# Kernel tuning notes

Hardware: AMD Instinct MI355X
Metric: run time of the kernel (lower is better)

## Reference

```python
import jax, jax.numpy as jnp
import numpy as np


def _block(x, a, b):
    # [..., W, H, D] -> [..., W//a, H//b, a, b, D]
    w, h, d = x.shape[-3:]
    x = jnp.reshape(x, x.shape[:-3] + (w // a, a, h // b, b, d))
    return jnp.moveaxis(x, -4, -3)


def _combine(x, bs):
    # [..., W, H, D] -> [..., W//bs, H//bs, bs*bs*D]
    x = _block(x, bs, bs)
    return jnp.reshape(x, x.shape[:-3] + (-1,))


def _normalize(x):
    x = x - jnp.mean(x, axis=-1, keepdims=True)
    return x / (jnp.linalg.norm(x, axis=-1, keepdims=True) + 1e-05)


def setup_inputs() -> dict:
    key = jax.random.key(0)
    k1, k2 = jax.random.split(key)
    x = jax.random.normal(k1, (8, 128, 128, 64), dtype=jnp.float32)
    y = jax.random.normal(k2, (8, 128, 128, 64), dtype=jnp.float32)
    return {"x": x, "y": y, "blocksize": 4}


def reference(x, y, blocksize):
    shape = x.shape
    xc = _normalize(_combine(x, blocksize))  # [B, W/bs, H/bs, F]
    yc = _normalize(_combine(y, blocksize))
    yf = jnp.reshape(yc, (-1, yc.shape[-1]))  # [M, F] codebook
    # single similarity matrix, reused for min-loss and argmax (original
    # computed jnp.inner twice -- same math)
    sim = jnp.einsum('...f,mf->...m', xc, yf)  # [B, W/bs, H/bs, M]
    cosloss = jnp.mean(jnp.min(1.0 - sim, axis=-1))
    idx = jnp.argmax(sim, axis=-1)
    # one-hot matmul against yf == top-1 gather (argmax picks first max, as
    # does the original I = (argmax - arange == 0) construction)
    new_x = jnp.take(yf, idx, axis=0)  # [B, W/bs, H/bs, F]
    new_x = jnp.reshape(new_x, new_x.shape[:-1] + (blocksize, blocksize, -1))
    new_x = jnp.swapaxes(new_x, -4, -3)
    new_x = jnp.reshape(new_x, shape)
    return cosloss, new_x
```

## Files before the change

kernel.cpp:

```cpp
#include <hip/hip_runtime.h>
#include <math.h>


#define NROWS 8192
#define KY 1024
#define NCH 64
#define EPS 3e-4f
#define FEPS 8e-4f

typedef _Float16 v8h __attribute__((ext_vector_type(8)));
typedef float f32x4 __attribute__((ext_vector_type(4)));

__device__ __forceinline__ unsigned umax(unsigned a, unsigned b) { return a > b ? a : b; }
__device__ __forceinline__ unsigned umin(unsigned a, unsigned b) { return a < b ? a : b; }

__device__ __forceinline__ unsigned packKey(float v, int col) {
    unsigned b = __float_as_uint(v);
    b ^= (unsigned)((int)b >> 31) | 0x80000000u;
    return (b & 0xFFFFE000u) | (unsigned)(8191 - col);
}

__device__ __forceinline__ float unpackApprox(unsigned k) {
    unsigned kb = k & 0xFFFFE000u;
    unsigned b = (kb & 0x80000000u) ? (kb ^ 0x80000000u) : ~kb;
    return __uint_as_float(b);
}

#define KMERGE(a1, a2, a3, b1, b2, b3) do {                                 \
    unsigned _n1 = umax(a1, b1);                                            \
    unsigned _n2 = umax(umin(a1, b1), umax(a2, b2));                        \
    unsigned _n3 = umax(umax(a3, b3), umax(umin(a1, b2), umin(a2, b1)));    \
    a1 = _n1; a2 = _n2; a3 = _n3;                                           \
} while (0)

__global__ __launch_bounds__(256) void normSplitKernel(
    const float* __restrict__ x, const float* __restrict__ y,
    _Float16* __restrict__ Xh, _Float16* __restrict__ Xl,
    _Float16* __restrict__ Yh, _Float16* __restrict__ Yl,
    int* __restrict__ flagCnt) {
    if (blockIdx.x == 0 && threadIdx.x == 0) *flagCnt = 0;
    int gr = blockIdx.x * 4 + (threadIdx.x >> 6);
    int ln = threadIdx.x & 63;
    bool isX = gr < NROWS;
    int row = isX ? gr : gr - NROWS;
    const float* src = isX ? x : y;
    _Float16* dh = isX ? Xh : Yh;
    _Float16* dl = isX ? Xl : Yl;
    int b = row >> 10, wq = (row >> 5) & 31, hq = row & 31;
    int a = ln >> 4, c = (ln >> 2) & 3, d0 = (ln & 3) << 4;
    const float* p = &src[(((size_t)(b * 128) + wq * 4 + a) * 128 + hq * 4 + c) * 64 + d0];
    float vv[16];
    *(float4*)(vv + 0)  = *(const float4*)(p + 0);
    *(float4*)(vv + 4)  = *(const float4*)(p + 4);
    *(float4*)(vv + 8)  = *(const float4*)(p + 8);
    *(float4*)(vv + 12) = *(const float4*)(p + 12);
    double s = 0.0;
    #pragma unroll
    for (int q = 0; q < 16; q++) s += (double)vv[q];
    #pragma unroll
    for (int m = 1; m < 64; m <<= 1) s += __shfl_xor(s, m, 64);
    double mean = s * (1.0 / 1024.0);
    double ss = 0.0;
    #pragma unroll
    for (int q = 0; q < 16; q++) {
        double d = (double)vv[q] - mean;
        ss += d * d;
    }
    #pragma unroll
    for (int m = 1; m < 64; m <<= 1) ss += __shfl_xor(ss, m, 64);
    double scale = 1.0 / (sqrt(ss) + 1e-5);
    _Float16 hi[16], lo[16];
    #pragma unroll
    for (int q = 0; q < 16; q++) {
        float f = (float)(((double)vv[q] - mean) * scale);
        _Float16 h = (_Float16)f;
        hi[q] = h;
        lo[q] = (_Float16)(f - (float)h);
    }
    size_t f0 = (size_t)row * KY + (ln << 4);
    *(v8h*)&dh[f0]     = *(v8h*)(hi);
    *(v8h*)&dh[f0 + 8] = *(v8h*)(hi + 8);
    *(v8h*)&dl[f0]     = *(v8h*)(lo);
    *(v8h*)&dl[f0 + 8] = *(v8h*)(lo + 8);
}

__global__ __launch_bounds__(256) void simKernel(
    const _Float16* __restrict__ Xh, const _Float16* __restrict__ Yh,
    float* __restrict__ pV1, unsigned* __restrict__ pK1,
    unsigned* __restrict__ pK2, unsigned* __restrict__ pK3) {
    __shared__ _Float16 As[2][128 * 32];
    __shared__ _Float16 Bs[2][128 * 32];
    __shared__ unsigned sK[2][2][64][3];
    __shared__ float sE[2][2][64];
    const int t = threadIdx.x;
    const int l = t & 63, w = t >> 6;
    const int wr = w >> 1, wc = w & 1;
    const int quad = l >> 4, lm = l & 15;
    const int flat = blockIdx.y * 64 + blockIdx.x;
    const int bx = flat >> 6, by = flat & 63;
    const int r0 = bx * 128, c0 = by * 128;

    f32x4 acc[4][4];
    #pragma unroll
    for (int i = 0; i < 4; i++)
        #pragma unroll
        for (int j = 0; j < 4; j++) acc[i][j] = (f32x4){0.f, 0.f, 0.f, 0.f};

    const _Float16* srcA0 = Xh + (size_t)(r0 + (t >> 2)) * KY + ((t & 3) << 3);
    const _Float16* srcA1 = srcA0 + (size_t)64 * KY;
    const _Float16* srcB0 = Yh + (size_t)(c0 + (t >> 2)) * KY + ((t & 3) << 3);
    const _Float16* srcB1 = srcB0 + (size_t)64 * KY;
    const int st8 = t * 8;

    {
        uint4 a0 = *(const uint4*)srcA0;
        uint4 a1 = *(const uint4*)srcA1;
        uint4 b0 = *(const uint4*)srcB0;
        uint4 b1 = *(const uint4*)srcB1;
        *(uint4*)&As[0][st8] = a0;
        *(uint4*)&As[0][2048 + st8] = a1;
        *(uint4*)&Bs[0][st8] = b0;
        *(uint4*)&Bs[0][2048 + st8] = b1;
    }
    __syncthreads();

    const int offA0 = (wr * 64 + lm) * 32 + quad * 8;
    const int offB0 = (wc * 64 + lm) * 32 + quad * 8;

    #pragma unroll 1
    for (int kk = 0; kk < KY - 32; kk += 32) {
        const int cur = (kk >> 5) & 1, nxt = cur ^ 1;
        const int kn = kk + 32;
        uint4 na0 = *(const uint4*)(srcA0 + kn);
        uint4 na1 = *(const uint4*)(srcA1 + kn);
        uint4 nb0 = *(const uint4*)(srcB0 + kn);
        uint4 nb1 = *(const uint4*)(srcB1 + kn);
        v8h af[4], bf[4];
        #pragma unroll
        for (int i = 0; i < 4; i++)
            af[i] = *(const v8h*)&As[cur][offA0 + i * 512];
        #pragma unroll
        for (int j = 0; j < 4; j++)
            bf[j] = *(const v8h*)&Bs[cur][offB0 + j * 512];
        #pragma unroll
        for (int i = 0; i < 4; i++)
            #pragma unroll
            for (int j = 0; j < 4; j++)
                acc[i][j] = __builtin_amdgcn_mfma_f32_16x16x32_f16(af[i], bf[j], acc[i][j], 0, 0, 0);
        *(uint4*)&As[nxt][st8] = na0;
        *(uint4*)&As[nxt][2048 + st8] = na1;
        *(uint4*)&Bs[nxt][st8] = nb0;
        *(uint4*)&Bs[nxt][2048 + st8] = nb1;
        __syncthreads();
    }
    {
        v8h af[4], bf[4];
        #pragma unroll
        for (int i = 0; i < 4; i++)
            af[i] = *(const v8h*)&As[1][offA0 + i * 512];
        #pragma unroll
        for (int j = 0; j < 4; j++)
            bf[j] = *(const v8h*)&Bs[1][offB0 + j * 512];
        #pragma unroll
        for (int i = 0; i < 4; i++)
            #pragma unroll
            for (int j = 0; j < 4; j++)
                acc[i][j] = __builtin_amdgcn_mfma_f32_16x16x32_f16(af[i], bf[j], acc[i][j], 0, 0, 0);
    }

    const int cbase = c0 + wc * 64 + lm;
    #pragma unroll
    for (int i = 0; i < 4; i++) {
        #pragma unroll
        for (int r = 0; r < 4; r++) {
            float v0 = acc[i][0][r], v1 = acc[i][1][r];
            float v2 = acc[i][2][r], v3 = acc[i][3][r];
            unsigned k0 = packKey(v0, cbase);
            unsigned k1 = packKey(v1, cbase + 16);
            unsigned k2 = packKey(v2, cbase + 32);
            unsigned k3 = packKey(v3, cbase + 48);
            unsigned h1 = umax(k0, k1), l1 = umin(k0, k1);
            unsigned h2 = umax(k2, k3), l2 = umin(k2, k3);
            unsigned a1 = umax(h1, h2);
            unsigned a2 = umax(umin(h1, h2), umax(l1, l2));
            unsigned a3 = umax(umin(h1, l2), umin(l1, h2));
            float ev = fmaxf(fmaxf(v0, v1), fmaxf(v2, v3));
            #pragma unroll
            for (int m = 1; m < 16; m <<= 1) {
                unsigned b1 = (unsigned)__shfl_xor((int)a1, m, 64);
                unsigned b2 = (unsigned)__shfl_xor((int)a2, m, 64);
                unsigned b3 = (unsigned)__shfl_xor((int)a3, m, 64);
                float be = __shfl_xor(ev, m, 64);
                KMERGE(a1, a2, a3, b1, b2, b3);
                ev = fmaxf(ev, be);
            }
            if (lm == 0) {
                int rr = i * 16 + quad * 4 + r;
                sK[wr][wc][rr][0] = a1; sK[wr][wc][rr][1] = a2; sK[wr][wc][rr][2] = a3;
                sE[wr][wc][rr] = ev;
            }
        }
    }
    __syncthreads();
    if (wc == 0) {
        unsigned a1 = sK[wr][0][l][0], a2 = sK[wr][0][l][1], a3 = sK[wr][0][l][2];
        unsigned b1 = sK[wr][1][l][0], b2 = sK[wr][1][l][1], b3 = sK[wr][1][l][2];
        KMERGE(a1, a2, a3, b1, b2, b3);
        float ev = fmaxf(sE[wr][0][l], sE[wr][1][l]);
        size_t o = (size_t)by * NROWS + (r0 + wr * 64 + l);
        pV1[o] = ev;
        pK1[o] = a1; pK2[o] = a2; pK3[o] = a3;
    }
}

__global__ __launch_bounds__(256) void reduceKernel(
    const float* __restrict__ pV1, const unsigned* __restrict__ pK1,
    const unsigned* __restrict__ pK2, const unsigned* __restrict__ pK3,
    int* __restrict__ bestIdx, int* __restrict__ flagRows,
    int* __restrict__ flagC2, int* __restrict__ flagC3,
    int* __restrict__ flagCnt, float* __restrict__ blkSum) {
    int t = threadIdx.x;
    int row = blockIdx.x * 256 + t;
    unsigned a1 = 0, a2 = 0, a3 = 0;
    float ev = -1e30f;
    for (int c = 0; c < NCH; c++) {
        size_t o = (size_t)c * NROWS + row;
        unsigned b1 = pK1[o], b2 = pK2[o], b3 = pK3[o];
        float e = pV1[o];
        KMERGE(a1, a2, a3, b1, b2, b3);
        ev = fmaxf(ev, e);
    }
    bestIdx[row] = 8191 - (int)(a1 & 8191u);
    if (ev - unpackApprox(a2) < FEPS) {
        int s = atomicAdd(flagCnt, 1);
        flagRows[s] = row;
        flagC2[s] = 8191 - (int)(a2 & 8191u);
        flagC3[s] = 8191 - (int)(a3 & 8191u);
    }
    double sum = 1.0 - (double)ev;
    __shared__ double sh[4];
    #pragma unroll
    for (int off = 32; off; off >>= 1) sum += __shfl_down(sum, off, 64);
    if ((t & 63) == 0) sh[t >> 6] = sum;
    __syncthreads();
    if (t == 0) blkSum[blockIdx.x] = (float)(sh[0] + sh[1] + sh[2] + sh[3]);
}

__global__ __launch_bounds__(256) void refineKernel(
    const _Float16* __restrict__ Xh, const _Float16* __restrict__ Xl,
    const _Float16* __restrict__ Yh, const _Float16* __restrict__ Yl,
    int* __restrict__ bestIdx, const int* __restrict__ flagRows,
    const int* __restrict__ flagC2, const int* __restrict__ flagC3,
    const int* __restrict__ flagCnt) {
    int n = *flagCnt;
    int wave = (blockIdx.x << 2) + (threadIdx.x >> 6);
    int ln = threadIdx.x & 63;
    for (int fi = wave; fi < n; fi += gridDim.x * 4) {
        int row = flagRows[fi];
        int cand[3];
        cand[0] = bestIdx[row]; cand[1] = flagC2[fi]; cand[2] = flagC3[fi];
        double d[3];
        #pragma unroll
        for (int c = 0; c < 3; c++) {
            double p = 0.0;
            int yr = cand[c];
            #pragma unroll
            for (int q = 0; q < 16; q++) {
                int k = (ln << 4) + q;
                float xv = (float)Xh[(size_t)row * KY + k] + (float)Xl[(size_t)row * KY + k];
                float yv = (float)Yh[(size_t)yr * KY + k] + (float)Yl[(size_t)yr * KY + k];
                p += (double)xv * yv;
            }
            #pragma unroll
            for (int m = 1; m < 64; m <<= 1) p += __shfl_xor(p, m, 64);
            d[c] = p;
        }
        if (ln == 0) {
            int bi = cand[0]; double bv = d[0];
            #pragma unroll
            for (int c = 1; c < 3; c++) {
                if (d[c] > bv || (d[c] == bv && cand[c] < bi)) { bv = d[c]; bi = cand[c]; }
            }
            bestIdx[row] = bi;
        }
    }
}

__global__ __launch_bounds__(256) void gatherKernel(
    const _Float16* __restrict__ Yh, const _Float16* __restrict__ Yl,
    const int* __restrict__ bestIdx, const float* __restrict__ blkSum,
    float* __restrict__ out) {
    int t = threadIdx.x;
    if (blockIdx.x == 0 && t == 0) {
        double s = 0.0;
        for (int i = 0; i < 32; i++) s += (double)blkSum[i];
        out[0] = (float)(s / 8192.0);
    }
    int g = (blockIdx.x * 256 + t) << 2;
    int b = g >> 20, wq = (g >> 13) & 127, hq = (g >> 6) & 127, d = g & 63;
    int row = (b << 10) + ((wq >> 2) << 5) + (hq >> 2);
    int f = ((wq & 3) << 8) + ((hq & 3) << 6) + d;
    size_t base = (size_t)bestIdx[row] * KY + f;
    const _Float16* ph = &Yh[base];
    const _Float16* pl = &Yl[base];
    out[1 + g + 0] = (float)ph[0] + (float)pl[0];
    out[1 + g + 1] = (float)ph[1] + (float)pl[1];
    out[1 + g + 2] = (float)ph[2] + (float)pl[2];
    out[1 + g + 3] = (float)ph[3] + (float)pl[3];
}

extern "C" void kernel_launch(void* const* d_in, const int* in_sizes, int n_in,
                              void* d_out, int out_size, void* d_ws, size_t ws_size,
                              hipStream_t stream) {
    const float* x = (const float*)d_in[0];
    const float* y = (const float*)d_in[1];
    float* out = (float*)d_out;
    char* ws = (char*)d_ws;
    _Float16* Xh  = (_Float16*)(ws);
    _Float16* Xl  = (_Float16*)(ws + 16777216u);
    _Float16* Yh  = (_Float16*)(ws + 33554432u);
    _Float16* Yl  = (_Float16*)(ws + 50331648u);
    float* pV1    = (float*)(ws + 67108864u);
    unsigned* pK1 = (unsigned*)(ws + 69206016u);
    unsigned* pK2 = (unsigned*)(ws + 71303168u);
    unsigned* pK3 = (unsigned*)(ws + 73400320u);
    int* bestIdx  = (int*)  (ws + 79691776u);
    int* flagRows = (int*)  (ws + 79724544u);
    int* flagC2   = (int*)  (ws + 79757312u);
    int* flagC3   = (int*)  (ws + 79790080u);
    int* flagCnt  = (int*)  (ws + 79822848u);
    float* blkSum = (float*)(ws + 79822976u);

    normSplitKernel<<<4096, 256, 0, stream>>>(x, y, Xh, Xl, Yh, Yl, flagCnt);
    simKernel<<<dim3(64, 64), 256, 0, stream>>>(Xh, Yh, pV1, pK1, pK2, pK3);
    reduceKernel<<<32, 256, 0, stream>>>(pV1, pK1, pK2, pK3,
                                         bestIdx, flagRows, flagC2, flagC3, flagCnt, blkSum);
    refineKernel<<<64, 256, 0, stream>>>(Xh, Xl, Yh, Yl, bestIdx,
                                         flagRows, flagC2, flagC3, flagCnt);
    gatherKernel<<<8192, 256, 0, stream>>>(Yh, Yl, bestIdx, blkSum, out);
}
```

Measured before the change: 356.4 us.

## Enlarge GEMM tiles to 256x256 with direct-to-LDS loads and swizzle

The similarity GEMM moves from 128x128 tiles with 256 threads to 256x256 tiles with 512 threads. Each wave computes a 128x64 sub-tile, which raises the reuse of each loaded fragment. Global-to-shared copies now use the global_load_lds intrinsic with an XOR swizzle, double buffering and explicit waitcnt/barrier scheduling plus setprio around the MFMA block. The number of column partials drops to 32, so the reduce kernel is reworked to use 4 lanes per row with shuffle merges across 128 blocks, and the final loss sum covers 128 block sums. The costs are higher register and LDS pressure and hand-written synchronisation that is fragile.

```diff
diff --git a/kernel.cpp b/kernel.cpp
--- a/kernel.cpp
+++ b/kernel.cpp
@@ -4,12 +4,18 @@
 
 #define NROWS 8192
 #define KY 1024
-#define NCH 64
+#define NCH 32
 #define EPS 3e-4f
 #define FEPS 8e-4f
 
 typedef _Float16 v8h __attribute__((ext_vector_type(8)));
 typedef float f32x4 __attribute__((ext_vector_type(4)));
+
+__device__ __forceinline__ void gload16(const _Float16* g, _Float16* l) {
+    __builtin_amdgcn_global_load_lds(
+        (const __attribute__((address_space(1))) void*)g,
+        (__attribute__((address_space(3))) void*)l, 16, 0, 0);
+}
 
 __device__ __forceinline__ unsigned umax(unsigned a, unsigned b) { return a > b ? a : b; }
 __device__ __forceinline__ unsigned umin(unsigned a, unsigned b) { return a < b ? a : b; }
@@ -84,93 +90,79 @@
     *(v8h*)&dl[f0 + 8] = *(v8h*)(lo + 8);
 }
 
-__global__ __launch_bounds__(256) void simKernel(
+__global__ __launch_bounds__(512, 2) void simKernel(
     const _Float16* __restrict__ Xh, const _Float16* __restrict__ Yh,
     float* __restrict__ pV1, unsigned* __restrict__ pK1,
     unsigned* __restrict__ pK2, unsigned* __restrict__ pK3) {
-    __shared__ _Float16 As[2][128 * 32];
-    __shared__ _Float16 Bs[2][128 * 32];
-    __shared__ unsigned sK[2][2][64][3];
-    __shared__ float sE[2][2][64];
+    __shared__ __align__(16) _Float16 As[2][256 * 32];
+    __shared__ __align__(16) _Float16 Bs[2][256 * 32];
+    __shared__ unsigned sK[2][4][128][3];
+    __shared__ float sE[2][4][128];
     const int t = threadIdx.x;
     const int l = t & 63, w = t >> 6;
-    const int wr = w >> 1, wc = w & 1;
+    const int wr = w >> 2, wc = w & 3;
     const int quad = l >> 4, lm = l & 15;
-    const int flat = blockIdx.y * 64 + blockIdx.x;
-    const int bx = flat >> 6, by = flat & 63;
-    const int r0 = bx * 128, c0 = by * 128;
-
-    f32x4 acc[4][4];
-    #pragma unroll
-    for (int i = 0; i < 4; i++)
+    const int flat = blockIdx.x;
+    const int bx = flat >> 5, by = flat & 31;
+    const int r0 = bx * 256, c0 = by * 256;
+
+    f32x4 acc[8][4];
+    #pragma unroll
+    for (int i = 0; i < 8; i++)
         #pragma unroll
         for (int j = 0; j < 4; j++) acc[i][j] = (f32x4){0.f, 0.f, 0.f, 0.f};
 
-    const _Float16* srcA0 = Xh + (size_t)(r0 + (t >> 2)) * KY + ((t & 3) << 3);
-    const _Float16* srcA1 = srcA0 + (size_t)64 * KY;
-    const _Float16* srcB0 = Yh + (size_t)(c0 + (t >> 2)) * KY + ((t & 3) << 3);
-    const _Float16* srcB1 = srcB0 + (size_t)64 * KY;
-    const int st8 = t * 8;
-
-    {
-        uint4 a0 = *(const uint4*)srcA0;
-        uint4 a1 = *(const uint4*)srcA1;
-        uint4 b0 = *(const uint4*)srcB0;
-        uint4 b1 = *(const uint4*)srcB1;
-        *(uint4*)&As[0][st8] = a0;
-        *(uint4*)&As[0][2048 + st8] = a1;
-        *(uint4*)&Bs[0][st8] = b0;
-        *(uint4*)&Bs[0][2048 + st8] = b1;
-    }
-    __syncthreads();
-
-    const int offA0 = (wr * 64 + lm) * 32 + quad * 8;
-    const int offB0 = (wc * 64 + lm) * 32 + quad * 8;
-
-    #pragma unroll 1
-    for (int kk = 0; kk < KY - 32; kk += 32) {
-        const int cur = (kk >> 5) & 1, nxt = cur ^ 1;
-        const int kn = kk + 32;
-        uint4 na0 = *(const uint4*)(srcA0 + kn);
-        uint4 na1 = *(const uint4*)(srcA1 + kn);
-        uint4 nb0 = *(const uint4*)(srcB0 + kn);
-        uint4 nb1 = *(const uint4*)(srcB1 + kn);
-        v8h af[4], bf[4];
-        #pragma unroll
-        for (int i = 0; i < 4; i++)
-            af[i] = *(const v8h*)&As[cur][offA0 + i * 512];
+    const int cq = l >> 2;
+    const int sA = (((l & 3) ^ (cq & 3)) << 3);
+    const _Float16* gA = Xh + (size_t)(r0 + w * 16 + cq) * KY + sA;
+    const _Float16* gB = Yh + (size_t)(c0 + w * 16 + cq) * KY + sA;
+    const int ldsBase = w * 512;
+
+#define STAGE(bb, kt) do {                                             \
+    const int _ko = (kt) * 32;                                         \
+    gload16(gA + _ko,                     &As[bb][ldsBase]);           \
+    gload16(gA + _ko + (size_t)128 * KY,  &As[bb][ldsBase + 4096]);    \
+    gload16(gB + _ko,                     &Bs[bb][ldsBase]);           \
+    gload16(gB + _ko + (size_t)128 * KY,  &Bs[bb][ldsBase + 4096]);    \
+} while (0)
+
+    const int swz = (quad ^ (lm & 3)) << 3;
+    const int offA0 = (wr * 128 + lm) * 32 + swz;
+    const int offB0 = (wc * 64 + lm) * 32 + swz;
+
+    STAGE(0, 0);
+    STAGE(1, 1);
+    asm volatile("s_waitcnt vmcnt(4)" ::: "memory");
+    __builtin_amdgcn_s_barrier();
+
+    #pragma unroll 2
+    for (int kt = 0; kt < 32; kt++) {
+        const int cur = kt & 1;
+        v8h af[8], bf[4];
+        #pragma unroll
+        for (int i = 0; i < 8; i++) af[i] = *(const v8h*)&As[cur][offA0 + i * 512];
+        #pragma unroll
+        for (int j = 0; j < 4; j++) bf[j] = *(const v8h*)&Bs[cur][offB0 + j * 512];
+        asm volatile("s_waitcnt lgkmcnt(0)" ::: "memory");
+        __builtin_amdgcn_sched_barrier(0);
+        __builtin_amdgcn_s_barrier();
+        STAGE(cur, (kt + 2) & 31);
+        __builtin_amdgcn_s_setprio(1);
         #pragma unroll
         for (int j = 0; j < 4; j++)
-            bf[j] = *(const v8h*)&Bs[cur][offB0 + j * 512];
-        #pragma unroll
-        for (int i = 0; i < 4; i++)
-            #pragma unroll
-            for (int j = 0; j < 4; j++)
+            #pragma unroll
+            for (int i = 0; i < 8; i++)
                 acc[i][j] = __builtin_amdgcn_mfma_f32_16x16x32_f16(af[i], bf[j], acc[i][j], 0, 0, 0);
-        *(uint4*)&As[nxt][st8] = na0;
-        *(uint4*)&As[nxt][2048 + st8] = na1;
-        *(uint4*)&Bs[nxt][st8] = nb0;
-        *(uint4*)&Bs[nxt][2048 + st8] = nb1;
-        __syncthreads();
-    }
-    {
-        v8h af[4], bf[4];
-        #pragma unroll
-        for (int i = 0; i < 4; i++)
-            af[i] = *(const v8h*)&As[1][offA0 + i * 512];
-        #pragma unroll
-        for (int j = 0; j < 4; j++)
-            bf[j] = *(const v8h*)&Bs[1][offB0 + j * 512];
-        #pragma unroll
-        for (int i = 0; i < 4; i++)
-            #pragma unroll
-            for (int j = 0; j < 4; j++)
-                acc[i][j] = __builtin_amdgcn_mfma_f32_16x16x32_f16(af[i], bf[j], acc[i][j], 0, 0, 0);
-    }
+        __builtin_amdgcn_s_setprio(0);
+        asm volatile("s_waitcnt vmcnt(4)" ::: "memory");
+        __builtin_amdgcn_s_barrier();
+    }
+    asm volatile("s_waitcnt vmcnt(0)" ::: "memory");
+#undef STAGE
 
     const int cbase = c0 + wc * 64 + lm;
     #pragma unroll
-    for (int i = 0; i < 4; i++) {
+    for (int i = 0; i < 8; i++) {
         #pragma unroll
         for (int r = 0; r < 4; r++) {
             float v0 = acc[i][0][r], v1 = acc[i][1][r];
@@ -202,12 +194,17 @@
         }
     }
     __syncthreads();
-    if (wc == 0) {
-        unsigned a1 = sK[wr][0][l][0], a2 = sK[wr][0][l][1], a3 = sK[wr][0][l][2];
-        unsigned b1 = sK[wr][1][l][0], b2 = sK[wr][1][l][1], b3 = sK[wr][1][l][2];
-        KMERGE(a1, a2, a3, b1, b2, b3);
-        float ev = fmaxf(sE[wr][0][l], sE[wr][1][l]);
-        size_t o = (size_t)by * NROWS + (r0 + wr * 64 + l);
+    if (t < 256) {
+        const int mwr = t >> 7, ri = t & 127;
+        unsigned a1 = sK[mwr][0][ri][0], a2 = sK[mwr][0][ri][1], a3 = sK[mwr][0][ri][2];
+        float ev = sE[mwr][0][ri];
+        #pragma unroll
+        for (int q = 1; q < 4; q++) {
+            unsigned b1 = sK[mwr][q][ri][0], b2 = sK[mwr][q][ri][1], b3 = sK[mwr][q][ri][2];
+            KMERGE(a1, a2, a3, b1, b2, b3);
+            ev = fmaxf(ev, sE[mwr][q][ri]);
+        }
+        size_t o = (size_t)by * NROWS + (r0 + t);
         pV1[o] = ev;
         pK1[o] = a1; pK2[o] = a2; pK3[o] = a3;
     }
@@ -220,24 +217,38 @@
     int* __restrict__ flagC2, int* __restrict__ flagC3,
     int* __restrict__ flagCnt, float* __restrict__ blkSum) {
     int t = threadIdx.x;
-    int row = blockIdx.x * 256 + t;
+    int g = blockIdx.x * 256 + t;
+    int row = g >> 2, sub = g & 3;
     unsigned a1 = 0, a2 = 0, a3 = 0;
     float ev = -1e30f;
-    for (int c = 0; c < NCH; c++) {
-        size_t o = (size_t)c * NROWS + row;
+    #pragma unroll
+    for (int k = 0; k < 8; k++) {
+        size_t o = (size_t)(sub + (k << 2)) * NROWS + row;
         unsigned b1 = pK1[o], b2 = pK2[o], b3 = pK3[o];
         float e = pV1[o];
         KMERGE(a1, a2, a3, b1, b2, b3);
         ev = fmaxf(ev, e);
     }
-    bestIdx[row] = 8191 - (int)(a1 & 8191u);
-    if (ev - unpackApprox(a2) < FEPS) {
-        int s = atomicAdd(flagCnt, 1);
-        flagRows[s] = row;
-        flagC2[s] = 8191 - (int)(a2 & 8191u);
-        flagC3[s] = 8191 - (int)(a3 & 8191u);
-    }
-    double sum = 1.0 - (double)ev;
+    #pragma unroll
+    for (int m = 1; m < 4; m <<= 1) {
+        unsigned b1 = (unsigned)__shfl_xor((int)a1, m, 64);
+        unsigned b2 = (unsigned)__shfl_xor((int)a2, m, 64);
+        unsigned b3 = (unsigned)__shfl_xor((int)a3, m, 64);
+        float be = __shfl_xor(ev, m, 64);
+        KMERGE(a1, a2, a3, b1, b2, b3);
+        ev = fmaxf(ev, be);
+    }
+    bool lead = (t & 3) == 0;
+    if (lead) {
+        bestIdx[row] = 8191 - (int)(a1 & 8191u);
+        if (ev - unpackApprox(a2) < FEPS) {
+            int s = atomicAdd(flagCnt, 1);
+            flagRows[s] = row;
+            flagC2[s] = 8191 - (int)(a2 & 8191u);
+            flagC3[s] = 8191 - (int)(a3 & 8191u);
+        }
+    }
+    double sum = lead ? 1.0 - (double)ev : 0.0;
     __shared__ double sh[4];
     #pragma unroll
     for (int off = 32; off; off >>= 1) sum += __shfl_down(sum, off, 64);
@@ -293,7 +304,7 @@
     int t = threadIdx.x;
     if (blockIdx.x == 0 && t == 0) {
         double s = 0.0;
-        for (int i = 0; i < 32; i++) s += (double)blkSum[i];
+        for (int i = 0; i < 128; i++) s += (double)blkSum[i];
         out[0] = (float)(s / 8192.0);
     }
     int g = (blockIdx.x * 256 + t) << 2;
@@ -332,9 +343,9 @@
     float* blkSum = (float*)(ws + 79822976u);
 
     normSplitKernel<<<4096, 256, 0, stream>>>(x, y, Xh, Xl, Yh, Yl, flagCnt);
-    simKernel<<<dim3(64, 64), 256, 0, stream>>>(Xh, Yh, pV1, pK1, pK2, pK3);
-    reduceKernel<<<32, 256, 0, stream>>>(pV1, pK1, pK2, pK3,
-                                         bestIdx, flagRows, flagC2, flagC3, flagCnt, blkSum);
+    simKernel<<<1024, 512, 0, stream>>>(Xh, Yh, pV1, pK1, pK2, pK3);
+    reduceKernel<<<128, 256, 0, stream>>>(pV1, pK1, pK2, pK3,
+                                          bestIdx, flagRows, flagC2, flagC3, flagCnt, blkSum);
     refineKernel<<<64, 256, 0, stream>>>(Xh, Xl, Yh, Yl, bestIdx,
                                          flagRows, flagC2, flagC3, flagCnt);
     gatherKernel<<<8192, 256, 0, stream>>>(Yh, Yl, bestIdx, blkSum, out);
```

New measurement: 328.8 us. -7.7%, faster.
